# Kernel tuning notes

Hardware: AMD Instinct MI355X
Metric: run time of the kernel (lower is better)

## Reference

```python
import jax, jax.numpy as jnp
import numpy as np

B, C, H, W = 8, 256, 128, 128
HEADS = 4
HEAD_DIM = C // HEADS  # 64
SCALE = HEAD_DIM ** -0.5


def setup_inputs() -> dict:
    key = jax.random.key(0)
    k1, k2, k3 = jax.random.split(key, 3)
    x = jax.random.normal(k1, (B, C, H, W), dtype=jnp.float32)
    # 1x1 convs == per-pixel linear layers; kaiming-ish small init
    Wqkv = jax.random.normal(k2, (3 * C, C), dtype=jnp.float32) * (1.0 / np.sqrt(C))
    bqkv = jnp.zeros((3 * C,), dtype=jnp.float32)
    Wproj = jax.random.normal(k3, (C, C), dtype=jnp.float32) * (1.0 / np.sqrt(C))
    bproj = jnp.zeros((C,), dtype=jnp.float32)
    return {"x": x, "Wqkv": Wqkv, "bqkv": bqkv, "Wproj": Wproj, "bproj": bproj}


def reference(x, Wqkv, bqkv, Wproj, bproj):
    b, c, h, w = x.shape
    hw = h * w
    xf = x.reshape(b, c, hw)  # [b, c, hw]
    # 1x1 conv QKV projection
    qkv = jnp.einsum('bcn,oc->bon', xf, Wqkv) + bqkv[None, :, None]  # [b, 3c, hw]
    qkv = qkv.reshape(b, 3, HEADS, HEAD_DIM, hw)
    q, k, v = qkv[:, 0], qkv[:, 1], qkv[:, 2]  # each [b, heads, d, hw]
    # channel attention: [b, heads, d, d]
    attn = jnp.einsum('bhdn,bhen->bhde', q, k) * SCALE
    attn = jax.nn.softmax(attn, axis=-1)
    out = jnp.einsum('bhde,bhen->bhdn', attn, v).reshape(b, c, hw)
    # output 1x1 conv
    out = jnp.einsum('bcn,oc->bon', out, Wproj) + bproj[None, :, None]
    return out.reshape(b, c, h, w)
```

## Files before the change

kernel.cpp:

```cpp
#include <hip/hip_runtime.h>
#include <hip/hip_bf16.h>
#include <stdint.h>


#define HW 16384
#define SCALE_F 0.125f
#define NF 16384.0f

typedef __attribute__((ext_vector_type(8))) short bf16x8;
typedef __attribute__((ext_vector_type(4))) float f32x4;

__device__ __forceinline__ unsigned short f2bf(float f) {
    union { float f; uint32_t u; } v; v.f = f;
    uint32_t u = v.u;
    return (unsigned short)((u + 0x7fffu + ((u >> 16) & 1u)) >> 16);
}
__device__ __forceinline__ float bf2f(unsigned short s) {
    union { uint32_t u; float f; } v; v.u = ((uint32_t)s) << 16;
    return v.f;
}
__device__ __forceinline__ uint32_t pk_bf16(float a, float b) {
    __hip_bfloat162 h = __float22bfloat162_rn(make_float2(a, b));
    union { __hip_bfloat162 h; uint32_t u; } c; c.h = h; return c.u;
}
__device__ __forceinline__ float ubf2f(uint32_t hibits) {
    union { uint32_t u; float f; } v; v.u = hibits; return v.f;
}

__global__ __launch_bounds__(512) void gram(
        const float* __restrict__ x, float* __restrict__ partG,
        float* __restrict__ parts_s) {
    const int kc = blockIdx.x;
    const int b  = blockIdx.y;
    __shared__ __align__(16) unsigned short Hs[2][256 * 32];
    __shared__ __align__(16) unsigned short Ls[2][256 * 32];
    const int tid = threadIdx.x, lane = tid & 63, w = tid >> 6;
    const int l15 = lane & 15, lg = lane >> 4;
    const int wr = w >> 1, wc = w & 1;
    const int srow = tid >> 1, shalf = tid & 1;
    const int m4 = (srow >> 1) & 3;
    const float* xb = x + (size_t)b * 256 * HW + (size_t)srow * HW + kc * 512 + shalf * 16;
    f32x4 acc[4][8] = {};
    float rs = 0.f;
    float4 ld[4];

#define LOADR(kstep)                                                            \
    {                                                                           \
        const float4* src = reinterpret_cast<const float4*>(xb + (kstep) * 32); \
        ld[0] = src[0]; ld[1] = src[1]; ld[2] = src[2]; ld[3] = src[3];         \
    }
#define STORE(sel)                                                              \
    {                                                                           \
        _Pragma("unroll")                                                       \
        for (int cq = 0; cq < 2; ++cq) {                                        \
            const float vv[8] = {ld[2*cq].x, ld[2*cq].y, ld[2*cq].z, ld[2*cq].w,\
                                 ld[2*cq+1].x, ld[2*cq+1].y, ld[2*cq+1].z, ld[2*cq+1].w}; \
            uint4 Hv, Lv;                                                       \
            uint32_t* Hp = reinterpret_cast<uint32_t*>(&Hv);                    \
            uint32_t* Lp = reinterpret_cast<uint32_t*>(&Lv);                    \
            _Pragma("unroll")                                                   \
            for (int p = 0; p < 4; ++p) {                                       \
                const float a0 = vv[2*p], a1 = vv[2*p+1];                       \
                const uint32_t hp = pk_bf16(a0, a1);                            \
                const float lo0 = a0 - ubf2f(hp << 16);                         \
                const float lo1 = a1 - ubf2f(hp & 0xffff0000u);                 \
                Hp[p] = hp;                                                     \
                Lp[p] = pk_bf16(lo0, lo1);                                      \
                rs += a0 + a1;                                                  \
            }                                                                   \
            const int slot = ((shalf * 2 + cq) ^ m4) << 4;                      \
            *reinterpret_cast<uint4*>((char*)(&Hs[sel][0]) + srow * 64 + slot) = Hv; \
            *reinterpret_cast<uint4*>((char*)(&Ls[sel][0]) + srow * 64 + slot) = Lv; \
        }                                                                       \
    }
#define DO_MFMA(sel)                                                            \
    {                                                                           \
        bf16x8 fah[4], fal[4];                                                  \
        _Pragma("unroll")                                                       \
        for (int i = 0; i < 4; ++i) {                                           \
            const int row = wr * 64 + i * 16 + l15;                             \
            const int off = row * 64 + ((lg ^ ((row >> 1) & 3)) << 4);          \
            fah[i] = *reinterpret_cast<const bf16x8*>((const char*)&Hs[sel][0] + off); \
            fal[i] = *reinterpret_cast<const bf16x8*>((const char*)&Ls[sel][0] + off); \
        }                                                                       \
        _Pragma("unroll")                                                       \
        for (int j = 0; j < 8; ++j) {                                           \
            const int row = wc * 128 + j * 16 + l15;                            \
            const int off = row * 64 + ((lg ^ ((row >> 1) & 3)) << 4);          \
            const bf16x8 fbh = *reinterpret_cast<const bf16x8*>((const char*)&Hs[sel][0] + off); \
            const bf16x8 fbl = *reinterpret_cast<const bf16x8*>((const char*)&Ls[sel][0] + off); \
            _Pragma("unroll")                                                   \
            for (int i = 0; i < 4; ++i) {                                       \
                acc[i][j] = __builtin_amdgcn_mfma_f32_16x16x32_bf16(fah[i], fbh, acc[i][j], 0, 0, 0); \
                acc[i][j] = __builtin_amdgcn_mfma_f32_16x16x32_bf16(fah[i], fbl, acc[i][j], 0, 0, 0); \
                acc[i][j] = __builtin_amdgcn_mfma_f32_16x16x32_bf16(fal[i], fbh, acc[i][j], 0, 0, 0); \
            }                                                                   \
        }                                                                       \
    }

    LOADR(0);
    STORE(0);
    __syncthreads();
    for (int t = 0; t < 16; ++t) {
        if (t < 15) LOADR(t + 1);
        DO_MFMA(t & 1);
        if (t < 15) STORE((t + 1) & 1);
        __syncthreads();
    }
#undef LOADR
#undef STORE
#undef DO_MFMA

    rs += __shfl_xor(rs, 1);
    if ((tid & 1) == 0) parts_s[(size_t)(b * 32 + kc) * 256 + srow] = rs;

    float* pw = partG + (size_t)(b * 32 + kc) * 65536;
    #pragma unroll
    for (int i = 0; i < 4; ++i)
        #pragma unroll
        for (int rr = 0; rr < 4; ++rr) {
            const int m = wr * 64 + i * 16 + lg * 4 + rr;
            #pragma unroll
            for (int j = 0; j < 8; ++j)
                pw[m * 256 + wc * 128 + j * 16 + l15] = acc[i][j][rr];
        }
}

__global__ __launch_bounds__(256) void greduce(
        const float4* __restrict__ partG4, float4* __restrict__ G4) {
    const int g = blockIdx.x * 256 + threadIdx.x;
    const int b = g >> 14, i4 = g & 16383;
    float4 a = make_float4(0.f, 0.f, 0.f, 0.f);
    #pragma unroll 8
    for (int kc = 0; kc < 32; ++kc) {
        const float4 v = partG4[(size_t)(b * 32 + kc) * 16384 + i4];
        a.x += v.x; a.y += v.y; a.z += v.z; a.w += v.w;
    }
    G4[g] = a;
}

__global__ __launch_bounds__(512) void tlogits(
        const float* __restrict__ G, const float* __restrict__ Wqkv,
        const float* __restrict__ bqkv, const float* __restrict__ parts_s,
        float* __restrict__ attn) {
    const int bh = blockIdx.x, b = bh >> 2, h = bh & 3;
    const int tid = threadIdx.x;
    __shared__ __align__(16) float SM[38528];
    float* R1 = SM;
    float* R2 = SM + 16896;
    float* WQ = SM + 33792;
    float* SB = SM + 38144;
    float* QS = SM + 38400;
    float* KS = SM + 38464;
    const float* Gb = G + (size_t)b * 65536;
    const float* Wq = Wqkv + (size_t)(h * 64) * 256;
    const float* Wk = Wqkv + (size_t)(256 + h * 64) * 256;

    if (tid < 256) {
        float a = 0.f;
        #pragma unroll
        for (int kc = 0; kc < 32; ++kc)
            a += parts_s[(size_t)(b * 32 + kc) * 256 + tid];
        SB[tid] = a;
    }
    {
        const int e = tid >> 3, cq = (tid & 7) * 32;
        #pragma unroll
        for (int q = 0; q < 8; ++q) {
            const float4 w4 = *reinterpret_cast<const float4*>(Wk + (size_t)e * 256 + cq + q * 4);
            R2[(cq + q * 4 + 0) * 66 + e] = w4.x;
            R2[(cq + q * 4 + 1) * 66 + e] = w4.y;
            R2[(cq + q * 4 + 2) * 66 + e] = w4.z;
            R2[(cq + q * 4 + 3) * 66 + e] = w4.w;
        }
    }
    __syncthreads();
    if (tid < 64) {
        float a = 0.f;
        for (int c = 0; c < 256; ++c) a += R2[c * 66 + tid] * SB[c];
        KS[tid] = a;
    }

    const int dq = tid >> 5, cb = tid & 31;
    float tacc[4][8] = {};
    float qacc = 0.f;
    for (int cc = 0; cc < 4; ++cc) {
        {
            const int r = tid >> 3, cq = (tid & 7) * 32;
            #pragma unroll
            for (int q = 0; q < 8; ++q)
                *reinterpret_cast<float4*>(&R1[r * 264 + cq + q * 4]) =
                    *reinterpret_cast<const float4*>(Gb + (size_t)(cc * 64 + r) * 256 + cq + q * 4);
        }
        {
            const int r = tid >> 3, c8 = (tid & 7) * 8;
            *reinterpret_cast<float4*>(&WQ[r * 68 + c8]) =
                *reinterpret_cast<const float4*>(Wq + (size_t)r * 256 + cc * 64 + c8);
            *reinterpret_cast<float4*>(&WQ[r * 68 + c8 + 4]) =
                *reinterpret_cast<const float4*>(Wq + (size_t)r * 256 + cc * 64 + c8 + 4);
        }
        __syncthreads();
        for (int c = 0; c < 64; ++c) {
            float wv[4];
            #pragma unroll
            for (int i = 0; i < 4; ++i) wv[i] = WQ[(dq * 4 + i) * 68 + c];
            #pragma unroll
            for (int jj = 0; jj < 8; ++jj) {
                const float gv = R1[c * 264 + cb + 32 * jj];
                #pragma unroll
                for (int i = 0; i < 4; ++i) tacc[i][jj] += wv[i] * gv;
            }
        }
        if (tid < 64) {
            float a = 0.f;
            for (int c = 0; c < 64; ++c) a += WQ[tid * 68 + c] * SB[cc * 64 + c];
            qacc += a;
        }
        __syncthreads();
    }
    if (tid < 64) QS[tid] = qacc;
    #pragma unroll
    for (int i = 0; i < 4; ++i)
        #pragma unroll
        for (int jj = 0; jj < 8; ++jj)
            R1[(dq * 4 + i) * 264 + cb + 32 * jj] = tacc[i][jj];
    __syncthreads();

    const int e2 = tid & 31;
    float lacc[4][2] = {};
    for (int c = 0; c < 256; ++c) {
        float tv[4];
        #pragma unroll
        for (int i = 0; i < 4; ++i) tv[i] = R1[(dq * 4 + i) * 264 + c];
        #pragma unroll
        for (int k = 0; k < 2; ++k) {
            const float wv = R2[c * 66 + e2 * 2 + k];
            #pragma unroll
            for (int i = 0; i < 4; ++i) lacc[i][k] += tv[i] * wv;
        }
    }
    float* lgs = WQ;
    const float* bq = bqkv + h * 64;
    const float* bk = bqkv + 256 + h * 64;
    #pragma unroll
    for (int i = 0; i < 4; ++i) {
        const int d = dq * 4 + i;
        #pragma unroll
        for (int k = 0; k < 2; ++k) {
            const int e = e2 * 2 + k;
            lgs[d * 65 + e] = SCALE_F * (lacc[i][k] + bq[d] * KS[e] + bk[e] * QS[d] + NF * bq[d] * bk[e]);
        }
    }
    __syncthreads();
    if (tid < 64) {
        float m = -1e30f;
        for (int e = 0; e < 64; ++e) m = fmaxf(m, lgs[tid * 65 + e]);
        float sum = 0.f;
        for (int e = 0; e < 64; ++e) {
            const float ex = __expf(lgs[tid * 65 + e] - m);
            sum += ex;
            lgs[tid * 65 + e] = ex;
        }
        const float inv = 1.f / sum;
        float* ar = attn + ((size_t)bh * 64 + tid) * 64;
        for (int e = 0; e < 64; ++e) ar[e] = lgs[tid * 65 + e] * inv;
    }
}

__global__ __launch_bounds__(256) void buildMP(
        const float* __restrict__ attn, const float* __restrict__ Wproj,
        const float* __restrict__ Wqkv, const float* __restrict__ bqkv,
        const float* __restrict__ bproj, unsigned short* __restrict__ P,
        float* __restrict__ cvec) {
    const int blk = blockIdx.x;
    const int b = blk >> 4, o0 = (blk & 15) * 16;
    const int tid = threadIdx.x;
    __shared__ __align__(16) float U[16512];
    __shared__ __align__(16) float WpL[16 * 258];
    __shared__ __align__(16) float ML[16 * 258];
    const int og = tid >> 6, cb = tid & 63;

    {
        const float* ab = attn + (size_t)b * 16384;
        #pragma unroll
        for (int q = 0; q < 16; ++q)
            *reinterpret_cast<float4*>(&U[tid * 64 + q * 4]) =
                *reinterpret_cast<const float4*>(ab + tid * 64 + q * 4);
    }
    {
        const int r = tid >> 4, cc = (tid & 15) * 16;
        #pragma unroll
        for (int q = 0; q < 4; ++q)
            *reinterpret_cast<float4*>(&WpL[r * 258 + cc + q * 4]) =
                *reinterpret_cast<const float4*>(Wproj + (size_t)(o0 + r) * 256 + cc + q * 4);
    }
    __syncthreads();

    float macc[4][4] = {};
    #pragma unroll
    for (int j = 0; j < 4; ++j)
        for (int d = 0; d < 64; ++d) {
            const float a = U[j * 4096 + d * 64 + cb];
            #pragma unroll
            for (int i = 0; i < 4; ++i)
                macc[i][j] += WpL[(og * 4 + i) * 258 + j * 64 + d] * a;
        }
    #pragma unroll
    for (int i = 0; i < 4; ++i)
        #pragma unroll
        for (int j = 0; j < 4; ++j)
            ML[(og * 4 + i) * 258 + j * 64 + cb] = macc[i][j];
    __syncthreads();

    if (tid < 16) {
        const int o = o0 + tid;
        float a = bproj[o];
        for (int he = 0; he < 256; ++he) a += ML[tid * 258 + he] * bqkv[512 + he];
        cvec[b * 256 + o] = a;
    }

    float pacc[4][4] = {};
    for (int ch = 0; ch < 4; ++ch) {
        {
            const int r = tid >> 2, cc = (tid & 3) * 64;
            #pragma unroll
            for (int q = 0; q < 16; ++q)
                *reinterpret_cast<float4*>(&U[r * 258 + cc + q * 4]) =
                    *reinterpret_cast<const float4*>(Wqkv + (size_t)(512 + ch * 64 + r) * 256 + cc + q * 4);
        }
        __syncthreads();
        for (int he = 0; he < 64; ++he) {
            float mw[4];
            #pragma unroll
            for (int i = 0; i < 4; ++i) mw[i] = ML[(og * 4 + i) * 258 + ch * 64 + he];
            #pragma unroll
            for (int j = 0; j < 4; ++j) {
                const float wv = U[he * 258 + j * 64 + cb];
                #pragma unroll
                for (int i = 0; i < 4; ++i) pacc[i][j] += mw[i] * wv;
            }
        }
        __syncthreads();
    }
    unsigned short* Pb = P + (size_t)b * 65536;
    #pragma unroll
    for (int i = 0; i < 4; ++i)
        #pragma unroll
        for (int j = 0; j < 4; ++j)
            Pb[(size_t)(o0 + og * 4 + i) * 256 + j * 64 + cb] = f2bf(pacc[i][j]);
}

__global__ __launch_bounds__(512) void out_gemm(
        const unsigned short* __restrict__ P, const float* __restrict__ x,
        const float* __restrict__ cvec, float* __restrict__ out) {
    const int n0 = blockIdx.x * 128;
    const int b  = blockIdx.y;
    __shared__ __align__(16) unsigned short Bs[8 * 128 * 32];
    const int tid = threadIdx.x, lane = tid & 63, w = tid >> 6;
    const int wr = w >> 1, wc = w & 1;
    const int l15 = lane & 15, lg = lane >> 4;
    const unsigned short* Pb = P + (size_t)b * 65536;

    {
        const int sn = tid & 127;
        const int sg = tid >> 7;
        const float* xcol = x + (size_t)b * 256 * HW + n0 + sn;
        float bv[64];
        #pragma unroll
        for (int s = 0; s < 8; ++s)
            #pragma unroll
            for (int i = 0; i < 8; ++i)
                bv[s * 8 + i] = xcol[(size_t)(s * 32 + sg * 8 + i) * HW];
        const int wslot = ((sg ^ ((sn >> 1) & 3)) << 4);
        #pragma unroll
        for (int s = 0; s < 8; ++s) {
            uint4 Bv;
            uint32_t* Bp = reinterpret_cast<uint32_t*>(&Bv);
            #pragma unroll
            for (int p = 0; p < 4; ++p)
                Bp[p] = pk_bf16(bv[s * 8 + 2 * p], bv[s * 8 + 2 * p + 1]);
            *reinterpret_cast<uint4*>((char*)Bs + s * 8192 + sn * 64 + wslot) = Bv;
        }
    }
    __syncthreads();

    f32x4 acc[4][4] = {};
    const int m4r = (l15 >> 1) & 3;
    bf16x8 fp0[4], fp1[4];
    #pragma unroll
    for (int i = 0; i < 4; ++i)
        fp0[i] = *reinterpret_cast<const bf16x8*>(
            Pb + (size_t)(wr * 64 + i * 16 + l15) * 256 + lg * 8);
    #pragma unroll
    for (int s = 0; s < 8; ++s) {
        bf16x8* cur = (s & 1) ? fp1 : fp0;
        bf16x8* nxt = (s & 1) ? fp0 : fp1;
        if (s < 7) {
            #pragma unroll
            for (int i = 0; i < 4; ++i)
                nxt[i] = *reinterpret_cast<const bf16x8*>(
                    Pb + (size_t)(wr * 64 + i * 16 + l15) * 256 + (s + 1) * 32 + lg * 8);
        }
        #pragma unroll
        for (int j = 0; j < 4; ++j) {
            const int row = wc * 64 + j * 16 + l15;
            const bf16x8 fx = *reinterpret_cast<const bf16x8*>(
                (const char*)Bs + s * 8192 + row * 64 + ((lg ^ m4r) << 4));
            #pragma unroll
            for (int i = 0; i < 4; ++i)
                acc[i][j] = __builtin_amdgcn_mfma_f32_16x16x32_bf16(fx, cur[i], acc[i][j], 0, 0, 0);
        }
    }

    float* ob = out + (size_t)b * 256 * HW;
    #pragma unroll
    for (int i = 0; i < 4; ++i) {
        const int m = wr * 64 + i * 16 + l15;
        const float bp = cvec[b * 256 + m];
        #pragma unroll
        for (int j = 0; j < 4; ++j) {
            const int n = n0 + wc * 64 + j * 16 + lg * 4;
            float4 o4;
            o4.x = acc[i][j][0] + bp;
            o4.y = acc[i][j][1] + bp;
            o4.z = acc[i][j][2] + bp;
            o4.w = acc[i][j][3] + bp;
            *reinterpret_cast<float4*>(ob + (size_t)m * HW + n) = o4;
        }
    }
}

extern "C" void kernel_launch(void* const* d_in, const int* in_sizes, int n_in,
                              void* d_out, int out_size, void* d_ws, size_t ws_size,
                              hipStream_t stream) {
    const float* x     = (const float*)d_in[0];
    const float* Wqkv  = (const float*)d_in[1];
    const float* bqkv  = (const float*)d_in[2];
    const float* Wproj = (const float*)d_in[3];
    const float* bproj = (const float*)d_in[4];
    float* out = (float*)d_out;

    char* ws = (char*)d_ws;
    float* partG   = (float*)(ws);
    float* G       = (float*)(ws + 67108864);
    float* attn    = (float*)(ws + 69206016);
    unsigned short* P = (unsigned short*)(ws + 69730304);
    float* cvec    = (float*)(ws + 70778880);
    float* parts_s = (float*)(ws + 70787072);

    gram    <<<dim3(32, 8),  512, 0, stream>>>(x, partG, parts_s);
    greduce <<<512,          256, 0, stream>>>((const float4*)partG, (float4*)G);
    tlogits <<<32,           512, 0, stream>>>(G, Wqkv, bqkv, parts_s, attn);
    buildMP <<<128,          256, 0, stream>>>(attn, Wproj, Wqkv, bqkv, bproj, P, cvec);
    out_gemm<<<dim3(128, 8), 512, 0, stream>>>(P, x, cvec, out);
}
```

Before: 211.1 us.

## Split tlogits across query-row quarters to launch more blocks

The logits kernel now splits each (batch, head) into four blocks of 16 query rows each, launching 128 blocks of 256 threads instead of 32 blocks of 512. Each block recomputes the full transposed Wk tile, the bias sums and the G tiles, but only its own slice of Wq·G and the logits and softmax. This spreads a small, latency-bound kernel over more compute units, at the cost of redundant G and Wk loads per block and less register blocking in the inner loops.

```diff
diff --git a/kernel.cpp b/kernel.cpp
--- a/kernel.cpp
+++ b/kernel.cpp
@@ -139,120 +139,101 @@
     G4[g] = a;
 }
 
-__global__ __launch_bounds__(512) void tlogits(
+__global__ __launch_bounds__(256) void tlogits(
         const float* __restrict__ G, const float* __restrict__ Wqkv,
         const float* __restrict__ bqkv, const float* __restrict__ parts_s,
         float* __restrict__ attn) {
-    const int bh = blockIdx.x, b = bh >> 2, h = bh & 3;
+    const int blk = blockIdx.x;
+    const int bh = blk >> 2, d0 = (blk & 3) * 16;
+    const int b = bh >> 2, h = bh & 3;
     const int tid = threadIdx.x;
-    __shared__ __align__(16) float SM[38528];
-    float* R1 = SM;
-    float* R2 = SM + 16896;
-    float* WQ = SM + 33792;
-    float* SB = SM + 38144;
-    float* QS = SM + 38400;
-    float* KS = SM + 38464;
+    __shared__ __align__(16) float WkT[256 * 68];
+    __shared__ __align__(16) float Gs[32 * 264];
+    __shared__ __align__(16) float Wqs[16 * 264];
+    __shared__ float lgs[16 * 65];
+    __shared__ float SB[256];
+    __shared__ float QS[16], KS[64];
     const float* Gb = G + (size_t)b * 65536;
-    const float* Wq = Wqkv + (size_t)(h * 64) * 256;
+    const float* Wq = Wqkv + (size_t)(h * 64 + d0) * 256;
     const float* Wk = Wqkv + (size_t)(256 + h * 64) * 256;
 
-    if (tid < 256) {
+    {
         float a = 0.f;
-        #pragma unroll
+        #pragma unroll 8
         for (int kc = 0; kc < 32; ++kc)
             a += parts_s[(size_t)(b * 32 + kc) * 256 + tid];
         SB[tid] = a;
     }
     {
-        const int e = tid >> 3, cq = (tid & 7) * 32;
-        #pragma unroll
-        for (int q = 0; q < 8; ++q) {
-            const float4 w4 = *reinterpret_cast<const float4*>(Wk + (size_t)e * 256 + cq + q * 4);
-            R2[(cq + q * 4 + 0) * 66 + e] = w4.x;
-            R2[(cq + q * 4 + 1) * 66 + e] = w4.y;
-            R2[(cq + q * 4 + 2) * 66 + e] = w4.z;
-            R2[(cq + q * 4 + 3) * 66 + e] = w4.w;
-        }
+        const int e = tid >> 2, cq = (tid & 3) * 64;
+        for (int q = 0; q < 64; q += 4) {
+            const float4 w4 = *reinterpret_cast<const float4*>(Wk + (size_t)e * 256 + cq + q);
+            WkT[(cq + q + 0) * 68 + e] = w4.x;
+            WkT[(cq + q + 1) * 68 + e] = w4.y;
+            WkT[(cq + q + 2) * 68 + e] = w4.z;
+            WkT[(cq + q + 3) * 68 + e] = w4.w;
+        }
+    }
+    {
+        const int r = tid >> 4, cq = (tid & 15) * 16;
+        #pragma unroll
+        for (int q = 0; q < 16; q += 4)
+            *reinterpret_cast<float4*>(&Wqs[r * 264 + cq + q]) =
+                *reinterpret_cast<const float4*>(Wq + (size_t)r * 256 + cq + q);
     }
     __syncthreads();
     if (tid < 64) {
         float a = 0.f;
-        for (int c = 0; c < 256; ++c) a += R2[c * 66 + tid] * SB[c];
+        for (int c = 0; c < 256; ++c) a += WkT[c * 68 + tid] * SB[c];
         KS[tid] = a;
-    }
-
-    const int dq = tid >> 5, cb = tid & 31;
-    float tacc[4][8] = {};
-    float qacc = 0.f;
-    for (int cc = 0; cc < 4; ++cc) {
+    } else if (tid >= 240) {
+        const int d = tid - 240;
+        float a = 0.f;
+        for (int c = 0; c < 256; ++c) a += Wqs[d * 264 + c] * SB[c];
+        QS[d] = a;
+    }
+
+    const int d = tid >> 4, cp0 = tid & 15;
+    float tacc[16] = {};
+    for (int cc = 0; cc < 8; ++cc) {
         {
             const int r = tid >> 3, cq = (tid & 7) * 32;
             #pragma unroll
-            for (int q = 0; q < 8; ++q)
-                *reinterpret_cast<float4*>(&R1[r * 264 + cq + q * 4]) =
-                    *reinterpret_cast<const float4*>(Gb + (size_t)(cc * 64 + r) * 256 + cq + q * 4);
-        }
-        {
-            const int r = tid >> 3, c8 = (tid & 7) * 8;
-            *reinterpret_cast<float4*>(&WQ[r * 68 + c8]) =
-                *reinterpret_cast<const float4*>(Wq + (size_t)r * 256 + cc * 64 + c8);
-            *reinterpret_cast<float4*>(&WQ[r * 68 + c8 + 4]) =
-                *reinterpret_cast<const float4*>(Wq + (size_t)r * 256 + cc * 64 + c8 + 4);
+            for (int q = 0; q < 32; q += 4)
+                *reinterpret_cast<float4*>(&Gs[r * 264 + cq + q]) =
+                    *reinterpret_cast<const float4*>(Gb + (size_t)(cc * 32 + r) * 256 + cq + q);
         }
         __syncthreads();
-        for (int c = 0; c < 64; ++c) {
-            float wv[4];
-            #pragma unroll
-            for (int i = 0; i < 4; ++i) wv[i] = WQ[(dq * 4 + i) * 68 + c];
-            #pragma unroll
-            for (int jj = 0; jj < 8; ++jj) {
-                const float gv = R1[c * 264 + cb + 32 * jj];
-                #pragma unroll
-                for (int i = 0; i < 4; ++i) tacc[i][jj] += wv[i] * gv;
-            }
-        }
-        if (tid < 64) {
-            float a = 0.f;
-            for (int c = 0; c < 64; ++c) a += WQ[tid * 68 + c] * SB[cc * 64 + c];
-            qacc += a;
+        for (int c = 0; c < 32; ++c) {
+            const float wv = Wqs[d * 264 + cc * 32 + c];
+            #pragma unroll
+            for (int j = 0; j < 16; ++j)
+                tacc[j] += wv * Gs[c * 264 + cp0 + 16 * j];
         }
         __syncthreads();
     }
-    if (tid < 64) QS[tid] = qacc;
-    #pragma unroll
-    for (int i = 0; i < 4; ++i)
-        #pragma unroll
-        for (int jj = 0; jj < 8; ++jj)
-            R1[(dq * 4 + i) * 264 + cb + 32 * jj] = tacc[i][jj];
-    __syncthreads();
-
-    const int e2 = tid & 31;
-    float lacc[4][2] = {};
+    #pragma unroll
+    for (int j = 0; j < 16; ++j)
+        Gs[d * 264 + cp0 + 16 * j] = tacc[j];
+    __syncthreads();
+
+    float lacc[4] = {};
+    const int e0 = (tid & 15) * 4;
     for (int c = 0; c < 256; ++c) {
-        float tv[4];
-        #pragma unroll
-        for (int i = 0; i < 4; ++i) tv[i] = R1[(dq * 4 + i) * 264 + c];
-        #pragma unroll
-        for (int k = 0; k < 2; ++k) {
-            const float wv = R2[c * 66 + e2 * 2 + k];
-            #pragma unroll
-            for (int i = 0; i < 4; ++i) lacc[i][k] += tv[i] * wv;
-        }
-    }
-    float* lgs = WQ;
-    const float* bq = bqkv + h * 64;
+        const float tv = Gs[d * 264 + c];
+        const float4 wv = *reinterpret_cast<const float4*>(&WkT[c * 68 + e0]);
+        lacc[0] += tv * wv.x; lacc[1] += tv * wv.y;
+        lacc[2] += tv * wv.z; lacc[3] += tv * wv.w;
+    }
+    const float* bq = bqkv + h * 64 + d0;
     const float* bk = bqkv + 256 + h * 64;
     #pragma unroll
-    for (int i = 0; i < 4; ++i) {
-        const int d = dq * 4 + i;
-        #pragma unroll
-        for (int k = 0; k < 2; ++k) {
-            const int e = e2 * 2 + k;
-            lgs[d * 65 + e] = SCALE_F * (lacc[i][k] + bq[d] * KS[e] + bk[e] * QS[d] + NF * bq[d] * bk[e]);
-        }
-    }
-    __syncthreads();
-    if (tid < 64) {
+    for (int k = 0; k < 4; ++k) {
+        const int e = e0 + k;
+        lgs[d * 65 + e] = SCALE_F * (lacc[k] + bq[d] * KS[e] + bk[e] * QS[d] + NF * bq[d] * bk[e]);
+    }
+    __syncthreads();
+    if (tid < 16) {
         float m = -1e30f;
         for (int e = 0; e < 64; ++e) m = fmaxf(m, lgs[tid * 65 + e]);
         float sum = 0.f;
@@ -262,7 +243,7 @@
             lgs[tid * 65 + e] = ex;
         }
         const float inv = 1.f / sum;
-        float* ar = attn + ((size_t)bh * 64 + tid) * 64;
+        float* ar = attn + ((size_t)bh * 64 + d0 + tid) * 64;
         for (int e = 0; e < 64; ++e) ar[e] = lgs[tid * 65 + e] * inv;
     }
 }
@@ -450,7 +431,7 @@
 
     gram    <<<dim3(32, 8),  512, 0, stream>>>(x, partG, parts_s);
     greduce <<<512,          256, 0, stream>>>((const float4*)partG, (float4*)G);
-    tlogits <<<32,           512, 0, stream>>>(G, Wqkv, bqkv, parts_s, attn);
+    tlogits <<<128,          256, 0, stream>>>(G, Wqkv, bqkv, parts_s, attn);
     buildMP <<<128,          256, 0, stream>>>(attn, Wproj, Wqkv, bqkv, bproj, P, cvec);
     out_gemm<<<dim3(128, 8), 512, 0, stream>>>(P, x, cvec, out);
 }
```

Measured after the change: 200.0 us (median of 2 runs). -5.3%, faster.
